# Kernel tuning notes

Measured on AMD Instinct MI355X. Metric: run time of the kernel, lower is better.

## Reference

```python
import jax, jax.numpy as jnp
import numpy as np
import math

NUM_HEADS = 8
HEAD_SIZE = 32

def get_alibi_slopes(n_heads):
    def pow2_slopes(n):
        start = 2.0 ** (-2.0 ** (-(math.log2(n) - 3)))
        ratio = start
        return [start * ratio ** i for i in range(n)]
    if math.log2(n_heads).is_integer():
        return np.array(pow2_slopes(n_heads), dtype=np.float32)
    cp2 = 2 ** math.floor(math.log2(n_heads))
    extra = pow2_slopes(2 * cp2)[0::2][: n_heads - cp2]
    return np.array(pow2_slopes(cp2) + extra, dtype=np.float32)

ALIBI_SLOPES = jnp.asarray(get_alibi_slopes(NUM_HEADS))  # [H]

def setup_inputs() -> dict:
    key = jax.random.key(0)
    ks = jax.random.split(key, 6)
    B, T, C = 32, 512, 256
    s = 1.0 / math.sqrt(C)
    return {
        "x": jax.random.normal(ks[0], (B, T, C), dtype=jnp.float32),
        "Wq": jax.random.normal(ks[1], (C, NUM_HEADS * HEAD_SIZE), dtype=jnp.float32) * s,
        "Wk": jax.random.normal(ks[2], (C, NUM_HEADS * HEAD_SIZE), dtype=jnp.float32) * s,
        "Wv": jax.random.normal(ks[3], (C, NUM_HEADS * HEAD_SIZE), dtype=jnp.float32) * s,
        "Wo": jax.random.normal(ks[4], (NUM_HEADS * HEAD_SIZE, C), dtype=jnp.float32) * s,
        "bo": jax.random.normal(ks[5], (C,), dtype=jnp.float32) * 0.01,
    }

def reference(x, Wq, Wk, Wv, Wo, bo):
    # Faithful eval-mode forward (dropout disabled) of the torch MultiHeadAttention.
    B, T, C = x.shape
    H, D = NUM_HEADS, HEAD_SIZE
    q = (x @ Wq).reshape(B, T, H, D).transpose(0, 2, 1, 3)  # [B,H,T,D]
    k = (x @ Wk).reshape(B, T, H, D).transpose(0, 2, 1, 3)
    v = (x @ Wv).reshape(B, T, H, D).transpose(0, 2, 1, 3)
    scale = 1.0 / math.sqrt(D)
    wei = jnp.einsum("bhtd,bhsd->bhts", q, k) * scale  # [B,H,T,T]
    pos = jnp.arange(T)
    rel = (pos[None, :] - pos[:, None]).astype(jnp.float32)  # bias[i,j] = j - i
    bias = ALIBI_SLOPES[:, None, None] * rel[None, :, :]      # [H,T,T]
    wei = wei + bias[None]
    causal = pos[None, :] <= pos[:, None]  # [T,T], True where j <= i
    wei = jnp.where(causal[None, None], wei, -jnp.inf)
    wei = jax.nn.softmax(wei, axis=-1)
    out = jnp.einsum("bhts,bhsd->bhtd", wei, v)  # [B,H,T,D]
    out = out.transpose(0, 2, 1, 3).reshape(B, T, H * D)
    return out @ Wo + bo
```

## Files before the change

kernel.cpp:

```cpp
#include <hip/hip_runtime.h>
#include <stdint.h>

#define LOG2E 1.4426950408889634f

typedef __attribute__((ext_vector_type(8))) short bf16x8;
typedef __attribute__((ext_vector_type(4))) float f32x4;

__device__ __forceinline__ unsigned short f2bf(float f) {
  union { float f; unsigned int u; } v; v.f = f;
  unsigned int u = v.u;
  u += 0x7FFFu + ((u >> 16) & 1u);
  return (unsigned short)(u >> 16);
}

__device__ __forceinline__ unsigned int cvt_pk_bf16(float lo, float hi) {
  unsigned int r;
  asm("v_cvt_pk_bf16_f32 %0, %1, %2" : "=v"(r) : "v"(lo), "v"(hi));
  return r;
}

struct WPtrs { const float* src[4]; unsigned short* dst[4]; };
__global__ void transpose_w(WPtrs p) {
  __shared__ float tile[32][33];
  const float* src = p.src[blockIdx.z];
  unsigned short* dst = p.dst[blockIdx.z];
  int x = blockIdx.x * 32 + threadIdx.x;
  int y = blockIdx.y * 32 + threadIdx.y;
  #pragma unroll
  for (int j = 0; j < 32; j += 8)
    tile[threadIdx.y + j][threadIdx.x] = src[(y + j) * 256 + x];
  __syncthreads();
  int xo = blockIdx.y * 32 + threadIdx.x;
  int yo = blockIdx.x * 32 + threadIdx.y;
  #pragma unroll
  for (int j = 0; j < 32; j += 8)
    dst[(yo + j) * 256 + xo] = f2bf(tile[threadIdx.x][threadIdx.y + j]);
}

template<int MODE>
__launch_bounds__(256, 3)
__global__ void gemm128(const float* __restrict__ Ax,
                        const unsigned short* __restrict__ Ab,
                        const unsigned short* __restrict__ Wt,
                        unsigned short* __restrict__ q_out,
                        unsigned short* __restrict__ k_out,
                        unsigned short* __restrict__ vT,
                        const float* __restrict__ bo,
                        float* __restrict__ f_out) {
  __shared__ unsigned short As[128][72];
  __shared__ unsigned short Bs[128][72];
  const int tid = threadIdx.x;
  const int m0 = blockIdx.x * 128;
  int wsel, n0;
  if (MODE == 0) { wsel = blockIdx.y >> 1; n0 = (blockIdx.y & 1) * 128; }
  else           { wsel = 0;               n0 = blockIdx.y * 128; }
  const unsigned short* W = Wt + wsel * 65536;
  const int w = tid >> 6, lane = tid & 63;
  const int wm = (w >> 1) * 64, wn = (w & 1) * 64;
  const int lr = lane & 15, lg = lane >> 4;

  f32x4 acc[4][4] = {};

  for (int kt = 0; kt < 4; ++kt) {
    #pragma unroll
    for (int cc = 0; cc < 4; ++cc) {
      int c = tid + cc * 256;
      int row = c >> 3, colg = c & 7;
      if constexpr (MODE == 0) {
        const float* s = &Ax[(size_t)(m0 + row) * 256 + kt * 64 + colg * 8];
        float4 f0 = *reinterpret_cast<const float4*>(s);
        float4 f1 = *reinterpret_cast<const float4*>(s + 4);
        uint4 pk;
        pk.x = cvt_pk_bf16(f0.x, f0.y); pk.y = cvt_pk_bf16(f0.z, f0.w);
        pk.z = cvt_pk_bf16(f1.x, f1.y); pk.w = cvt_pk_bf16(f1.z, f1.w);
        *reinterpret_cast<uint4*>(&As[row][colg * 8]) = pk;
      } else {
        *reinterpret_cast<int4*>(&As[row][colg * 8]) =
          *reinterpret_cast<const int4*>(&Ab[(size_t)(m0 + row) * 256 + kt * 64 + colg * 8]);
      }
      *reinterpret_cast<int4*>(&Bs[row][colg * 8]) =
        *reinterpret_cast<const int4*>(&W[(size_t)(n0 + row) * 256 + kt * 64 + colg * 8]);
    }
    __syncthreads();
    #pragma unroll
    for (int kk = 0; kk < 2; ++kk) {
      bf16x8 af[4], bfr[4];
      #pragma unroll
      for (int mf = 0; mf < 4; ++mf)
        af[mf] = *reinterpret_cast<const bf16x8*>(&As[wm + mf * 16 + lr][kk * 32 + lg * 8]);
      #pragma unroll
      for (int nf = 0; nf < 4; ++nf)
        bfr[nf] = *reinterpret_cast<const bf16x8*>(&Bs[wn + nf * 16 + lr][kk * 32 + lg * 8]);
      #pragma unroll
      for (int mf = 0; mf < 4; ++mf)
        #pragma unroll
        for (int nf = 0; nf < 4; ++nf)
          acc[mf][nf] = __builtin_amdgcn_mfma_f32_16x16x32_bf16(af[mf], bfr[nf], acc[mf][nf], 0, 0, 0);
    }
    __syncthreads();
  }

  if (MODE == 0) {
    if (wsel < 2) {
      unsigned short* dst = (wsel == 0) ? q_out : k_out;
      #pragma unroll
      for (int mf = 0; mf < 4; ++mf)
        #pragma unroll
        for (int nf = 0; nf < 4; ++nf)
          #pragma unroll
          for (int r = 0; r < 4; ++r)
            dst[(size_t)(m0 + wm + mf * 16 + lg * 4 + r) * 256 + (n0 + wn + nf * 16 + lr)] =
              f2bf(acc[mf][nf][r]);
    } else {
      #pragma unroll
      for (int mf = 0; mf < 4; ++mf)
        #pragma unroll
        for (int nf = 0; nf < 4; ++nf) {
          int ncol = n0 + wn + nf * 16 + lr;
          int h = ncol >> 5, d = ncol & 31;
          int m = m0 + wm + mf * 16 + lg * 4;
          int b = m >> 9, t = m & 511;
          ushort4 pk;
          pk.x = f2bf(acc[mf][nf][0]); pk.y = f2bf(acc[mf][nf][1]);
          pk.z = f2bf(acc[mf][nf][2]); pk.w = f2bf(acc[mf][nf][3]);
          *reinterpret_cast<ushort4*>(&vT[((size_t)((b * 8 + h) * 32 + d)) * 512 + t]) = pk;
        }
    }
  } else {
    #pragma unroll
    for (int mf = 0; mf < 4; ++mf)
      #pragma unroll
      for (int nf = 0; nf < 4; ++nf)
        #pragma unroll
        for (int r = 0; r < 4; ++r) {
          int ncol = n0 + wn + nf * 16 + lr;
          f_out[(size_t)(m0 + wm + mf * 16 + lg * 4 + r) * 256 + ncol] = acc[mf][nf][r] + bo[ncol];
        }
  }
}

struct CSt {
  bf16x8 qf;
  f32x4 o0, o1;
  float m, l, bb0;
  int nfull, qq;
};

__device__ __forceinline__ void attn_init(CSt& st, int c, const unsigned short* qb,
    int b, int h, int lr, int lg, float slope2) {
  st.qq = c * 16;
  st.qf = *reinterpret_cast<const bf16x8*>(
      &qb[(size_t)(b * 512 + st.qq + lr) * 256 + h * 32 + lg * 8]);
  f32x4 z = {0.f, 0.f, 0.f, 0.f};
  st.o0 = z; st.o1 = z;
  st.m = -1e30f; st.l = 0.f;
  st.nfull = (st.qq >= 63) ? ((st.qq - 63) / 64 + 1) : 0;
  st.bb0 = slope2 * (float)(lg * 4 - lr - st.qq);
}

__device__ __forceinline__ void attn_step(CSt& st, int s,
    const unsigned short* __restrict__ Ks, const unsigned short* __restrict__ Vs,
    char* __restrict__ Pw, int lr, int lg, float scale2, float slope2,
    const float* cc, int swz) {
  const int kb0 = s * 64;
  const int kchunk = (lg ^ ((lr >> 1) & 3)) * 8;
  f32x4 sv[4];
  #pragma unroll
  for (int t = 0; t < 4; ++t) {
    bf16x8 kf = *reinterpret_cast<const bf16x8*>(&Ks[(kb0 + t * 16 + lr) * 32 + kchunk]);
    f32x4 z = {0.f, 0.f, 0.f, 0.f};
    sv[t] = __builtin_amdgcn_mfma_f32_16x16x32_bf16(kf, st.qf, z, 0, 0, 0);
  }
  float bb = st.bb0 + slope2 * (float)kb0;
  float x[16];
  #pragma unroll
  for (int t = 0; t < 4; ++t)
    #pragma unroll
    for (int r = 0; r < 4; ++r)
      x[t * 4 + r] = sv[t][r] * scale2 + (bb + cc[t * 4 + r]);
  if (s >= st.nfull) {
    int thr = st.qq + lr - kb0 - lg * 4;
    #pragma unroll
    for (int t = 0; t < 4; ++t)
      #pragma unroll
      for (int r = 0; r < 4; ++r)
        x[t * 4 + r] = ((t * 16 + r) <= thr) ? x[t * 4 + r] : -1e30f;
  }
  float bm = x[0];
  #pragma unroll
  for (int j = 1; j < 16; ++j) bm = fmaxf(bm, x[j]);
  bm = fmaxf(bm, __shfl_xor(bm, 16));
  bm = fmaxf(bm, __shfl_xor(bm, 32));
  float mn = fmaxf(st.m, bm);
  float alpha = __builtin_amdgcn_exp2f(st.m - mn);
  st.m = mn;
  st.l *= alpha;
  #pragma unroll
  for (int r = 0; r < 4; ++r) { st.o0[r] *= alpha; st.o1[r] *= alpha; }
  float ps = 0.f;
  #pragma unroll
  for (int j = 0; j < 16; ++j) { x[j] = __builtin_amdgcn_exp2f(x[j] - mn); ps += x[j]; }
  st.l += ps;
  char* Prow = Pw + lr * 128;
  #pragma unroll
  for (int t = 0; t < 4; ++t)
    #pragma unroll
    for (int pp = 0; pp < 2; ++pp) {
      unsigned int w2 = cvt_pk_bf16(x[t * 4 + 2 * pp], x[t * 4 + 2 * pp + 1]);
      *reinterpret_cast<unsigned int*>(Prow + ((t * 32 + lg * 8 + pp * 4) ^ swz)) = w2;
    }
  #pragma unroll
  for (int ks = 0; ks < 2; ++ks) {
    bf16x8 pb = *reinterpret_cast<const bf16x8*>(Prow + ((ks * 64 + lg * 16) ^ swz));
    #pragma unroll
    for (int dt = 0; dt < 2; ++dt) {
      int col = (kb0 + ks * 32 + lg * 8) ^ ((lr & 7) << 3);
      bf16x8 vf = *reinterpret_cast<const bf16x8*>(&Vs[(dt * 16 + lr) * 512 + col]);
      if (dt == 0) st.o0 = __builtin_amdgcn_mfma_f32_16x16x32_bf16(vf, pb, st.o0, 0, 0, 0);
      else         st.o1 = __builtin_amdgcn_mfma_f32_16x16x32_bf16(vf, pb, st.o1, 0, 0, 0);
    }
  }
}

__device__ __forceinline__ void attn_fin(CSt& st, unsigned short* __restrict__ ob,
                                         int b, int h, int lr, int lg) {
  float l = st.l;
  l += __shfl_xor(l, 16);
  l += __shfl_xor(l, 32);
  float inv = 1.0f / l;
  unsigned int w0 = cvt_pk_bf16(st.o0[0] * inv, st.o0[1] * inv);
  unsigned int w1 = cvt_pk_bf16(st.o0[2] * inv, st.o0[3] * inv);
  unsigned int w2 = cvt_pk_bf16(st.o1[0] * inv, st.o1[1] * inv);
  unsigned int w3 = cvt_pk_bf16(st.o1[2] * inv, st.o1[3] * inv);
  size_t obase = (size_t)(b * 512 + st.qq + lr) * 256 + h * 32;
  *reinterpret_cast<uint2*>(&ob[obase + lg * 4]) = make_uint2(w0, w1);
  *reinterpret_cast<uint2*>(&ob[obase + 16 + lg * 4]) = make_uint2(w2, w3);
}

__launch_bounds__(256, 2)
__global__ void attn_k(const unsigned short* __restrict__ qb,
                       const unsigned short* __restrict__ kb,
                       const unsigned short* __restrict__ vT,
                       unsigned short* __restrict__ ob) {
  __shared__ unsigned short Ks[512 * 32];
  __shared__ unsigned short Vs[32 * 512];
  __shared__ char Pb[8192];
  const int p = blockIdx.x, h = blockIdx.y, b = blockIdx.z;
  const int tid = threadIdx.x, wv = tid >> 6, lane = tid & 63;
  const int lr = lane & 15, lg = lane >> 4;

  {
    const unsigned short* ksrc = kb + ((size_t)b * 512) * 256 + h * 32;
    #pragma unroll
    for (int it = 0; it < 8; ++it) {
      int idx = tid + it * 256;
      int row = idx >> 2, g = idx & 3;
      int gs = g ^ ((row >> 1) & 3);
      *reinterpret_cast<int4*>(&Ks[row * 32 + gs * 8]) =
        *reinterpret_cast<const int4*>(&ksrc[(size_t)row * 256 + g * 8]);
    }
    const unsigned short* vsrc = vT + ((size_t)(b * 8 + h) * 32) * 512;
    #pragma unroll
    for (int it = 0; it < 8; ++it) {
      int idx = tid + it * 256;
      int d = idx >> 6, cg = idx & 63;
      int col = (cg * 8) ^ ((d & 7) << 3);
      *reinterpret_cast<int4*>(&Vs[d * 512 + col]) =
        *reinterpret_cast<const int4*>(&vsrc[(size_t)d * 512 + cg * 8]);
    }
  }
  __syncthreads();

  const float scale2 = 0.17677669529663687f * LOG2E;
  const float slope2 = exp2f(-(float)(h + 1)) * LOG2E;
  float cc[16];
  #pragma unroll
  for (int t = 0; t < 4; ++t)
    #pragma unroll
    for (int r = 0; r < 4; ++r) cc[t * 4 + r] = slope2 * (float)(t * 16 + r);
  const int swz = (lr & 7) << 4;
  char* Pw = Pb + wv * 2048;

  const int g = p * 4 + wv;
  const int c0 = g, c1 = 15 - g, c2 = 16 + g, c3 = 31 - g;
  CSt s0, s1, s2, s3;
  attn_init(s0, c0, qb, b, h, lr, lg, slope2);
  attn_init(s1, c1, qb, b, h, lr, lg, slope2);
  attn_init(s2, c2, qb, b, h, lr, lg, slope2);
  attn_init(s3, c3, qb, b, h, lr, lg, slope2);
  const int n0 = c0 / 4 + 1, n1 = c1 / 4 + 1, n2 = c2 / 4 + 1, n3 = c3 / 4 + 1;

  for (int s = 0; s < n3; ++s) {
    if (s < n0) attn_step(s0, s, Ks, Vs, Pw, lr, lg, scale2, slope2, cc, swz);
    if (s < n1) attn_step(s1, s, Ks, Vs, Pw, lr, lg, scale2, slope2, cc, swz);
    if (s < n2) attn_step(s2, s, Ks, Vs, Pw, lr, lg, scale2, slope2, cc, swz);
    attn_step(s3, s, Ks, Vs, Pw, lr, lg, scale2, slope2, cc, swz);
  }

  attn_fin(s0, ob, b, h, lr, lg);
  attn_fin(s1, ob, b, h, lr, lg);
  attn_fin(s2, ob, b, h, lr, lg);
  attn_fin(s3, ob, b, h, lr, lg);
}

extern "C" void kernel_launch(void* const* d_in, const int* in_sizes, int n_in,
                              void* d_out, int out_size, void* d_ws, size_t ws_size,
                              hipStream_t stream) {
  const float* x  = (const float*)d_in[0];
  const float* Wq = (const float*)d_in[1];
  const float* Wk = (const float*)d_in[2];
  const float* Wv = (const float*)d_in[3];
  const float* Wo = (const float*)d_in[4];
  const float* bo = (const float*)d_in[5];
  float* out = (float*)d_out;

  char* ws = (char*)d_ws;
  unsigned short* qb = (unsigned short*)(ws);
  unsigned short* kb = (unsigned short*)(ws + (8u  << 20));
  unsigned short* vT = (unsigned short*)(ws + (16u << 20));
  unsigned short* ob = (unsigned short*)(ws + (24u << 20));
  unsigned short* wt = (unsigned short*)(ws + (32u << 20));

  WPtrs p;
  p.src[0] = Wq; p.src[1] = Wk; p.src[2] = Wv; p.src[3] = Wo;
  p.dst[0] = wt; p.dst[1] = wt + 65536; p.dst[2] = wt + 2 * 65536; p.dst[3] = wt + 3 * 65536;
  transpose_w<<<dim3(8, 8, 4), dim3(32, 8), 0, stream>>>(p);

  gemm128<0><<<dim3(128, 6), 256, 0, stream>>>(x, nullptr, wt, qb, kb, vT, nullptr, nullptr);
  attn_k<<<dim3(2, 8, 32), 256, 0, stream>>>(qb, kb, vT, ob);
  gemm128<1><<<dim3(128, 2), 256, 0, stream>>>(nullptr, ob, wt + 3 * 65536, nullptr, nullptr, nullptr, bo, out);
}
```

Before: 58.46 us.

## Retile QKV GEMM to 64x256 and share K/V fragments across attention chunks

The QKV projection becomes a dedicated kernel with 64-row by 256-column tiles, so each block covers a full weight matrix and converts each x tile once per weight instead of twice. In attention, the K and V fragments for each 64-key step are loaded from LDS once and reused by all four query chunks, rather than reloaded inside every step. The P scratch buffer is doubled so alternating chunks write to separate halves, which reduces write-after-read hazards between consecutive steps. The cost is more registers per wave and more shared memory per block, which could reduce occupancy.

```diff
diff --git a/kernel.cpp b/kernel.cpp
--- a/kernel.cpp
+++ b/kernel.cpp
@@ -37,24 +37,100 @@
     dst[(yo + j) * 256 + xo] = f2bf(tile[threadIdx.x][threadIdx.y + j]);
 }
 
-template<int MODE>
 __launch_bounds__(256, 3)
-__global__ void gemm128(const float* __restrict__ Ax,
-                        const unsigned short* __restrict__ Ab,
-                        const unsigned short* __restrict__ Wt,
-                        unsigned short* __restrict__ q_out,
-                        unsigned short* __restrict__ k_out,
-                        unsigned short* __restrict__ vT,
-                        const float* __restrict__ bo,
-                        float* __restrict__ f_out) {
+__global__ void gemm_qkv(const float* __restrict__ Ax,
+                         const unsigned short* __restrict__ Wt,
+                         unsigned short* __restrict__ q_out,
+                         unsigned short* __restrict__ k_out,
+                         unsigned short* __restrict__ vT) {
+  __shared__ unsigned short As[64][72];
+  __shared__ unsigned short Bs[256][72];
+  const int tid = threadIdx.x;
+  const int m0 = blockIdx.x * 64;
+  const int wsel = blockIdx.y;
+  const unsigned short* W = Wt + wsel * 65536;
+  const int w = tid >> 6, lane = tid & 63;
+  const int n0 = w * 64;
+  const int lr = lane & 15, lg = lane >> 4;
+
+  f32x4 acc[4][4] = {};
+
+  for (int kt = 0; kt < 4; ++kt) {
+    #pragma unroll
+    for (int i = 0; i < 2; ++i) {
+      int c = tid + i * 256;
+      int row = c >> 3, colg = c & 7;
+      const float* s = &Ax[(size_t)(m0 + row) * 256 + kt * 64 + colg * 8];
+      float4 f0 = *reinterpret_cast<const float4*>(s);
+      float4 f1 = *reinterpret_cast<const float4*>(s + 4);
+      uint4 pk;
+      pk.x = cvt_pk_bf16(f0.x, f0.y); pk.y = cvt_pk_bf16(f0.z, f0.w);
+      pk.z = cvt_pk_bf16(f1.x, f1.y); pk.w = cvt_pk_bf16(f1.z, f1.w);
+      *reinterpret_cast<uint4*>(&As[row][colg * 8]) = pk;
+    }
+    #pragma unroll
+    for (int i = 0; i < 8; ++i) {
+      int c = tid + i * 256;
+      int row = c >> 3, colg = c & 7;
+      *reinterpret_cast<int4*>(&Bs[row][colg * 8]) =
+        *reinterpret_cast<const int4*>(&W[(size_t)row * 256 + kt * 64 + colg * 8]);
+    }
+    __syncthreads();
+    #pragma unroll
+    for (int kk = 0; kk < 2; ++kk) {
+      bf16x8 af[4], bfr[4];
+      #pragma unroll
+      for (int mf = 0; mf < 4; ++mf)
+        af[mf] = *reinterpret_cast<const bf16x8*>(&As[mf * 16 + lr][kk * 32 + lg * 8]);
+      #pragma unroll
+      for (int nf = 0; nf < 4; ++nf)
+        bfr[nf] = *reinterpret_cast<const bf16x8*>(&Bs[n0 + nf * 16 + lr][kk * 32 + lg * 8]);
+      #pragma unroll
+      for (int mf = 0; mf < 4; ++mf)
+        #pragma unroll
+        for (int nf = 0; nf < 4; ++nf)
+          acc[mf][nf] = __builtin_amdgcn_mfma_f32_16x16x32_bf16(af[mf], bfr[nf], acc[mf][nf], 0, 0, 0);
+    }
+    __syncthreads();
+  }
+
+  if (wsel < 2) {
+    unsigned short* dst = (wsel == 0) ? q_out : k_out;
+    #pragma unroll
+    for (int mf = 0; mf < 4; ++mf)
+      #pragma unroll
+      for (int nf = 0; nf < 4; ++nf)
+        #pragma unroll
+        for (int r = 0; r < 4; ++r)
+          dst[(size_t)(m0 + mf * 16 + lg * 4 + r) * 256 + (n0 + nf * 16 + lr)] =
+            f2bf(acc[mf][nf][r]);
+  } else {
+    #pragma unroll
+    for (int mf = 0; mf < 4; ++mf)
+      #pragma unroll
+      for (int nf = 0; nf < 4; ++nf) {
+        int ncol = n0 + nf * 16 + lr;
+        int h = ncol >> 5, d = ncol & 31;
+        int m = m0 + mf * 16 + lg * 4;
+        int b = m >> 9, t = m & 511;
+        ushort4 pk;
+        pk.x = f2bf(acc[mf][nf][0]); pk.y = f2bf(acc[mf][nf][1]);
+        pk.z = f2bf(acc[mf][nf][2]); pk.w = f2bf(acc[mf][nf][3]);
+        *reinterpret_cast<ushort4*>(&vT[((size_t)((b * 8 + h) * 32 + d)) * 512 + t]) = pk;
+      }
+  }
+}
+
+__launch_bounds__(256, 3)
+__global__ void gemm_out(const unsigned short* __restrict__ Ab,
+                         const unsigned short* __restrict__ W,
+                         const float* __restrict__ bo,
+                         float* __restrict__ f_out) {
   __shared__ unsigned short As[128][72];
   __shared__ unsigned short Bs[128][72];
   const int tid = threadIdx.x;
   const int m0 = blockIdx.x * 128;
-  int wsel, n0;
-  if (MODE == 0) { wsel = blockIdx.y >> 1; n0 = (blockIdx.y & 1) * 128; }
-  else           { wsel = 0;               n0 = blockIdx.y * 128; }
-  const unsigned short* W = Wt + wsel * 65536;
+  const int n0 = blockIdx.y * 128;
   const int w = tid >> 6, lane = tid & 63;
   const int wm = (w >> 1) * 64, wn = (w & 1) * 64;
   const int lr = lane & 15, lg = lane >> 4;
@@ -66,18 +142,8 @@
     for (int cc = 0; cc < 4; ++cc) {
       int c = tid + cc * 256;
       int row = c >> 3, colg = c & 7;
-      if constexpr (MODE == 0) {
-        const float* s = &Ax[(size_t)(m0 + row) * 256 + kt * 64 + colg * 8];
-        float4 f0 = *reinterpret_cast<const float4*>(s);
-        float4 f1 = *reinterpret_cast<const float4*>(s + 4);
-        uint4 pk;
-        pk.x = cvt_pk_bf16(f0.x, f0.y); pk.y = cvt_pk_bf16(f0.z, f0.w);
-        pk.z = cvt_pk_bf16(f1.x, f1.y); pk.w = cvt_pk_bf16(f1.z, f1.w);
-        *reinterpret_cast<uint4*>(&As[row][colg * 8]) = pk;
-      } else {
-        *reinterpret_cast<int4*>(&As[row][colg * 8]) =
-          *reinterpret_cast<const int4*>(&Ab[(size_t)(m0 + row) * 256 + kt * 64 + colg * 8]);
-      }
+      *reinterpret_cast<int4*>(&As[row][colg * 8]) =
+        *reinterpret_cast<const int4*>(&Ab[(size_t)(m0 + row) * 256 + kt * 64 + colg * 8]);
       *reinterpret_cast<int4*>(&Bs[row][colg * 8]) =
         *reinterpret_cast<const int4*>(&W[(size_t)(n0 + row) * 256 + kt * 64 + colg * 8]);
     }
@@ -100,43 +166,15 @@
     __syncthreads();
   }
 
-  if (MODE == 0) {
-    if (wsel < 2) {
-      unsigned short* dst = (wsel == 0) ? q_out : k_out;
-      #pragma unroll
-      for (int mf = 0; mf < 4; ++mf)
-        #pragma unroll
-        for (int nf = 0; nf < 4; ++nf)
-          #pragma unroll
-          for (int r = 0; r < 4; ++r)
-            dst[(size_t)(m0 + wm + mf * 16 + lg * 4 + r) * 256 + (n0 + wn + nf * 16 + lr)] =
-              f2bf(acc[mf][nf][r]);
-    } else {
-      #pragma unroll
-      for (int mf = 0; mf < 4; ++mf)
-        #pragma unroll
-        for (int nf = 0; nf < 4; ++nf) {
-          int ncol = n0 + wn + nf * 16 + lr;
-          int h = ncol >> 5, d = ncol & 31;
-          int m = m0 + wm + mf * 16 + lg * 4;
-          int b = m >> 9, t = m & 511;
-          ushort4 pk;
-          pk.x = f2bf(acc[mf][nf][0]); pk.y = f2bf(acc[mf][nf][1]);
-          pk.z = f2bf(acc[mf][nf][2]); pk.w = f2bf(acc[mf][nf][3]);
-          *reinterpret_cast<ushort4*>(&vT[((size_t)((b * 8 + h) * 32 + d)) * 512 + t]) = pk;
-        }
-    }
-  } else {
-    #pragma unroll
-    for (int mf = 0; mf < 4; ++mf)
-      #pragma unroll
-      for (int nf = 0; nf < 4; ++nf)
-        #pragma unroll
-        for (int r = 0; r < 4; ++r) {
-          int ncol = n0 + wn + nf * 16 + lr;
-          f_out[(size_t)(m0 + wm + mf * 16 + lg * 4 + r) * 256 + ncol] = acc[mf][nf][r] + bo[ncol];
-        }
-  }
+  #pragma unroll
+  for (int mf = 0; mf < 4; ++mf)
+    #pragma unroll
+    for (int nf = 0; nf < 4; ++nf)
+      #pragma unroll
+      for (int r = 0; r < 4; ++r) {
+        int ncol = n0 + wn + nf * 16 + lr;
+        f_out[(size_t)(m0 + wm + mf * 16 + lg * 4 + r) * 256 + ncol] = acc[mf][nf][r] + bo[ncol];
+      }
 }
 
 struct CSt {
@@ -159,17 +197,14 @@
 }
 
 __device__ __forceinline__ void attn_step(CSt& st, int s,
-    const unsigned short* __restrict__ Ks, const unsigned short* __restrict__ Vs,
-    char* __restrict__ Pw, int lr, int lg, float scale2, float slope2,
-    const float* cc, int swz) {
+    const bf16x8* kf, const bf16x8* vf, char* __restrict__ Pw,
+    int lr, int lg, float scale2, float slope2, const float* cc, int swz) {
   const int kb0 = s * 64;
-  const int kchunk = (lg ^ ((lr >> 1) & 3)) * 8;
   f32x4 sv[4];
   #pragma unroll
   for (int t = 0; t < 4; ++t) {
-    bf16x8 kf = *reinterpret_cast<const bf16x8*>(&Ks[(kb0 + t * 16 + lr) * 32 + kchunk]);
     f32x4 z = {0.f, 0.f, 0.f, 0.f};
-    sv[t] = __builtin_amdgcn_mfma_f32_16x16x32_bf16(kf, st.qf, z, 0, 0, 0);
+    sv[t] = __builtin_amdgcn_mfma_f32_16x16x32_bf16(kf[t], st.qf, z, 0, 0, 0);
   }
   float bb = st.bb0 + slope2 * (float)kb0;
   float x[16];
@@ -212,13 +247,8 @@
   #pragma unroll
   for (int ks = 0; ks < 2; ++ks) {
     bf16x8 pb = *reinterpret_cast<const bf16x8*>(Prow + ((ks * 64 + lg * 16) ^ swz));
-    #pragma unroll
-    for (int dt = 0; dt < 2; ++dt) {
-      int col = (kb0 + ks * 32 + lg * 8) ^ ((lr & 7) << 3);
-      bf16x8 vf = *reinterpret_cast<const bf16x8*>(&Vs[(dt * 16 + lr) * 512 + col]);
-      if (dt == 0) st.o0 = __builtin_amdgcn_mfma_f32_16x16x32_bf16(vf, pb, st.o0, 0, 0, 0);
-      else         st.o1 = __builtin_amdgcn_mfma_f32_16x16x32_bf16(vf, pb, st.o1, 0, 0, 0);
-    }
+    st.o0 = __builtin_amdgcn_mfma_f32_16x16x32_bf16(vf[ks * 2 + 0], pb, st.o0, 0, 0, 0);
+    st.o1 = __builtin_amdgcn_mfma_f32_16x16x32_bf16(vf[ks * 2 + 1], pb, st.o1, 0, 0, 0);
   }
 }
 
@@ -244,7 +274,7 @@
                        unsigned short* __restrict__ ob) {
   __shared__ unsigned short Ks[512 * 32];
   __shared__ unsigned short Vs[32 * 512];
-  __shared__ char Pb[8192];
+  __shared__ char Pb[16384];
   const int p = blockIdx.x, h = blockIdx.y, b = blockIdx.z;
   const int tid = threadIdx.x, wv = tid >> 6, lane = tid & 63;
   const int lr = lane & 15, lg = lane >> 4;
@@ -279,7 +309,9 @@
     #pragma unroll
     for (int r = 0; r < 4; ++r) cc[t * 4 + r] = slope2 * (float)(t * 16 + r);
   const int swz = (lr & 7) << 4;
-  char* Pw = Pb + wv * 2048;
+  const int kchunk = (lg ^ ((lr >> 1) & 3)) * 8;
+  char* Pw0 = Pb + wv * 4096;
+  char* Pw1 = Pw0 + 2048;
 
   const int g = p * 4 + wv;
   const int c0 = g, c1 = 15 - g, c2 = 16 + g, c3 = 31 - g;
@@ -291,10 +323,23 @@
   const int n0 = c0 / 4 + 1, n1 = c1 / 4 + 1, n2 = c2 / 4 + 1, n3 = c3 / 4 + 1;
 
   for (int s = 0; s < n3; ++s) {
-    if (s < n0) attn_step(s0, s, Ks, Vs, Pw, lr, lg, scale2, slope2, cc, swz);
-    if (s < n1) attn_step(s1, s, Ks, Vs, Pw, lr, lg, scale2, slope2, cc, swz);
-    if (s < n2) attn_step(s2, s, Ks, Vs, Pw, lr, lg, scale2, slope2, cc, swz);
-    attn_step(s3, s, Ks, Vs, Pw, lr, lg, scale2, slope2, cc, swz);
+    const int kb0 = s * 64;
+    bf16x8 kf[4], vf[4];
+    #pragma unroll
+    for (int t = 0; t < 4; ++t)
+      kf[t] = *reinterpret_cast<const bf16x8*>(&Ks[(kb0 + t * 16 + lr) * 32 + kchunk]);
+    #pragma unroll
+    for (int ks = 0; ks < 2; ++ks)
+      #pragma unroll
+      for (int dt = 0; dt < 2; ++dt) {
+        int d = dt * 16 + lr;
+        int col = (kb0 + ks * 32 + lg * 8) ^ ((d & 7) << 3);
+        vf[ks * 2 + dt] = *reinterpret_cast<const bf16x8*>(&Vs[d * 512 + col]);
+      }
+    if (s < n0) attn_step(s0, s, kf, vf, Pw0, lr, lg, scale2, slope2, cc, swz);
+    if (s < n1) attn_step(s1, s, kf, vf, Pw1, lr, lg, scale2, slope2, cc, swz);
+    if (s < n2) attn_step(s2, s, kf, vf, Pw0, lr, lg, scale2, slope2, cc, swz);
+    attn_step(s3, s, kf, vf, Pw1, lr, lg, scale2, slope2, cc, swz);
   }
 
   attn_fin(s0, ob, b, h, lr, lg);
@@ -326,7 +371,7 @@
   p.dst[0] = wt; p.dst[1] = wt + 65536; p.dst[2] = wt + 2 * 65536; p.dst[3] = wt + 3 * 65536;
   transpose_w<<<dim3(8, 8, 4), dim3(32, 8), 0, stream>>>(p);
 
-  gemm128<0><<<dim3(128, 6), 256, 0, stream>>>(x, nullptr, wt, qb, kb, vT, nullptr, nullptr);
+  gemm_qkv<<<dim3(256, 3), 256, 0, stream>>>(x, wt, qb, kb, vT);
   attn_k<<<dim3(2, 8, 32), 256, 0, stream>>>(qb, kb, vT, ob);
-  gemm128<1><<<dim3(128, 2), 256, 0, stream>>>(nullptr, ob, wt + 3 * 65536, nullptr, nullptr, nullptr, bo, out);
-}
+  gemm_out<<<dim3(128, 2), 256, 0, stream>>>(ob, wt + 3 * 65536, bo, out);
+}
```

New measurement: 58.70 us. No clear change (+0.4%).
